# Optimization experiments

Hardware: AMD Instinct MI355X
Metric: run time of the kernel (lower is better)

## Reference

```python
import jax, jax.numpy as jnp
import numpy as np

B, S, H = 16, 4096, 1024

def setup_inputs() -> dict:
    key = jax.random.key(0)
    k1, k2, k3, k4, k5 = jax.random.split(key, 5)
    x = jax.random.normal(k1, (B, S, H), dtype=jnp.float32)
    lengths = jax.random.randint(k2, (B,), 1, S + 1, dtype=jnp.int32)
    W = jax.random.normal(k3, (H, H), dtype=jnp.float32) * (1.0 / np.sqrt(H))
    b = jax.random.normal(k4, (H,), dtype=jnp.float32) * 0.01
    key_vec = jax.random.normal(k5, (H,), dtype=jnp.float32)
    return {"x": x, "lengths": lengths, "W": W, "b": b, "key_vec": key_vec}

def reference(x, lengths, W, b, key_vec):
    # query = tanh(Linear(x)) : [B,S,H]
    query = jnp.tanh(jnp.einsum('bsh,oh->bso', x, W) + b)
    # scores = query @ key_vec : [B,S]
    scores = jnp.einsum('bsh,h->bs', query, key_vec)
    # masked softmax over valid positions (equivalent to per-sample slice softmax)
    seq_len = x.shape[1]
    valid = jnp.arange(seq_len)[None, :] < lengths[:, None]  # [B,S]
    scores = jnp.where(valid, scores, -jnp.inf)
    attn = jax.nn.softmax(scores, axis=-1)  # masked positions get 0
    # weighted sum of x : [B,H]
    return jnp.einsum('bs,bsh->bh', attn, x)
```

## Files before the change

### kernel.cpp

```cpp
#include <hip/hip_runtime.h>
#include <math.h>

#define BB 16
#define SS 4096
#define HH 1024
#define SCH 64


typedef __attribute__((ext_vector_type(8))) short bf16x8;
typedef __attribute__((ext_vector_type(16))) float f32x16;

__device__ __forceinline__ void gl_lds16(const void* g, void* l) {
  __builtin_amdgcn_global_load_lds(
      (const __attribute__((address_space(1))) void*)g,
      (__attribute__((address_space(3))) void*)l, 16, 0, 0);
}

__global__ __launch_bounds__(256) void conv_w(const float* __restrict__ W,
                                              unsigned short* __restrict__ Bbuf) {
  int ct = blockIdx.x, kc = blockIdx.y;
  unsigned short* blk = Bbuf + (size_t)(ct * 32 + kc) * 8192;
  int tid = threadIdx.x;
#pragma unroll
  for (int it = 0; it < 16; ++it) {
    int flat = it * 256 + tid;
    int n = flat >> 5, kk = flat & 31;
    float f = W[(size_t)(ct * 128 + n) * HH + kc * 32 + kk];
    unsigned u = __float_as_uint(f);
    float hf = __uint_as_float(u & 0xffff0000u);
    blk[n * 32 + kk] = (unsigned short)(u >> 16);
    blk[4096 + n * 32 + kk] = (unsigned short)(__float_as_uint(f - hf) >> 16);
  }
}

__global__ __launch_bounds__(256, 2) void scores_gemm(
    const float* __restrict__ x, const int* __restrict__ lengths,
    const unsigned short* __restrict__ Bbuf, const float* __restrict__ bias,
    const float* __restrict__ key, float* __restrict__ scores) {
  int ct = blockIdx.x;
  int t = blockIdx.y;
  int b = t >> 5;
  int s0 = (t & 31) * 128;
  if (s0 >= lengths[b]) return;

  __shared__ char lds[32768];
  int tid = threadIdx.x;
  int lane = tid & 63, w = tid >> 6;
  int wm = w & 1, wn = w >> 1;

  f32x16 acc[2][2];
#pragma unroll
  for (int mt = 0; mt < 2; ++mt)
#pragma unroll
    for (int nt = 0; nt < 2; ++nt)
#pragma unroll
      for (int i = 0; i < 16; ++i) acc[mt][nt][i] = 0.f;

  const float* xb = x + ((size_t)b * SS + s0) * HH;
  const char* Bblk0 = (const char*)Bbuf + (size_t)ct * 32 * 16384;

  int ar = tid >> 3;
  int ak = (tid & 7) * 4;

  int mrow = lane & 31;
  int khsel = lane >> 5;
  char* aP = lds + (wm * 64 + mrow) * 64 + khsel * 16;
  char* bP = lds + 16384 + (wn * 64 + mrow) * 64 + khsel * 16;

  for (int kc = 0; kc < 32; ++kc) {
    const char* Bblk = Bblk0 + kc * 16384;
#pragma unroll
    for (int i = 0; i < 4; ++i) {
      int c = w * 4 + i;
      gl_lds16(Bblk + c * 1024 + lane * 16, lds + 16384 + c * 1024);
    }
#pragma unroll
    for (int it = 0; it < 4; ++it) {
      int r = ar + it * 32;
      float4 v = *(const float4*)(xb + (size_t)r * HH + kc * 32 + ak);
      unsigned u0 = __float_as_uint(v.x), u1 = __float_as_uint(v.y);
      unsigned u2 = __float_as_uint(v.z), u3 = __float_as_uint(v.w);
      float l0 = v.x - __uint_as_float(u0 & 0xffff0000u);
      float l1 = v.y - __uint_as_float(u1 & 0xffff0000u);
      float l2 = v.z - __uint_as_float(u2 & 0xffff0000u);
      float l3 = v.w - __uint_as_float(u3 & 0xffff0000u);
      uint2 hp, lp;
      hp.x = (u0 >> 16) | (u1 & 0xffff0000u);
      hp.y = (u2 >> 16) | (u3 & 0xffff0000u);
      lp.x = (__float_as_uint(l0) >> 16) | (__float_as_uint(l1) & 0xffff0000u);
      lp.y = (__float_as_uint(l2) >> 16) | (__float_as_uint(l3) & 0xffff0000u);
      *(uint2*)(lds + r * 64 + ak * 2) = hp;
      *(uint2*)(lds + 8192 + r * 64 + ak * 2) = lp;
    }
    __syncthreads();

#pragma unroll
    for (int kh = 0; kh < 2; ++kh) {
      bf16x8 ah[2], al[2], bh[2], bl[2];
#pragma unroll
      for (int mt = 0; mt < 2; ++mt) {
        ah[mt] = *(bf16x8*)(aP + mt * 2048 + kh * 32);
        al[mt] = *(bf16x8*)(aP + 8192 + mt * 2048 + kh * 32);
        bh[mt] = *(bf16x8*)(bP + mt * 2048 + kh * 32);
        bl[mt] = *(bf16x8*)(bP + 8192 + mt * 2048 + kh * 32);
      }
#pragma unroll
      for (int mt = 0; mt < 2; ++mt)
#pragma unroll
        for (int nt = 0; nt < 2; ++nt) {
          acc[mt][nt] = __builtin_amdgcn_mfma_f32_32x32x16_bf16(
              ah[mt], bh[nt], acc[mt][nt], 0, 0, 0);
          acc[mt][nt] = __builtin_amdgcn_mfma_f32_32x32x16_bf16(
              ah[mt], bl[nt], acc[mt][nt], 0, 0, 0);
          acc[mt][nt] = __builtin_amdgcn_mfma_f32_32x32x16_bf16(
              al[mt], bh[nt], acc[mt][nt], 0, 0, 0);
        }
    }
    __syncthreads();
  }

  int col = lane & 31;
  int rbase = (lane >> 5) * 4;
  float bo[2], ko[2];
#pragma unroll
  for (int nt = 0; nt < 2; ++nt) {
    int o = ct * 128 + wn * 64 + nt * 32 + col;
    bo[nt] = bias[o];
    ko[nt] = key[o];
  }
  float* srow = scores + (size_t)b * SS + s0;
#pragma unroll
  for (int mt = 0; mt < 2; ++mt) {
#pragma unroll
    for (int reg = 0; reg < 16; ++reg) {
      float sv = tanhf(acc[mt][0][reg] + bo[0]) * ko[0] +
                 tanhf(acc[mt][1][reg] + bo[1]) * ko[1];
#pragma unroll
      for (int off = 1; off < 32; off <<= 1) sv += __shfl_xor(sv, off);
      if (col == 0) {
        int row = wm * 64 + mt * 32 + (reg & 3) + 8 * (reg >> 2) + rbase;
        atomicAdd(srow + row, sv);
      }
    }
  }
}

__global__ __launch_bounds__(256) void softmax_kernel(float* __restrict__ sc,
                                                      const int* __restrict__ lengths) {
  int b = blockIdx.x;
  int L = lengths[b];
  float* p = sc + (size_t)b * SS;
  __shared__ float sred[34];
  int tid = threadIdx.x;

  float m = -3.0e38f;
  for (int s = tid; s < L; s += 256) m = fmaxf(m, p[s]);
  for (int off = 32; off > 0; off >>= 1) m = fmaxf(m, __shfl_down(m, off));
  if ((tid & 63) == 0) sred[tid >> 6] = m;
  __syncthreads();
  if (tid == 0) {
    float mm = sred[0];
    for (int w = 1; w < 4; ++w) mm = fmaxf(mm, sred[w]);
    sred[32] = mm;
  }
  __syncthreads();
  m = sred[32];

  float z = 0.f;
  for (int s = tid; s < L; s += 256) z += expf(p[s] - m);
  for (int off = 32; off > 0; off >>= 1) z += __shfl_down(z, off);
  if ((tid & 63) == 0) sred[tid >> 6] = z;
  __syncthreads();
  if (tid == 0) {
    float zz = 0.f;
    for (int w = 0; w < 4; ++w) zz += sred[w];
    sred[33] = zz;
  }
  __syncthreads();
  float inv = 1.f / sred[33];
  for (int s = tid; s < L; s += 256) p[s] = expf(p[s] - m) * inv;
}

__global__ __launch_bounds__(256) void wsum_kernel(const float* __restrict__ x,
                                                   const float* __restrict__ p,
                                                   const int* __restrict__ lengths,
                                                   float* __restrict__ out) {
  int b = blockIdx.y;
  int L = lengths[b];
  int sbeg = blockIdx.x * SCH;
  if (sbeg >= L) return;
  int send = min(sbeg + SCH, L);
  int h = threadIdx.x * 4;
  const float* xb = x + (size_t)b * SS * HH;
  const float* pb = p + (size_t)b * SS;
  float4 acc = {0.f, 0.f, 0.f, 0.f};
  for (int s = sbeg; s < send; ++s) {
    float wgt = pb[s];
    float4 v = *(const float4*)(xb + (size_t)s * HH + h);
    acc.x = fmaf(wgt, v.x, acc.x);
    acc.y = fmaf(wgt, v.y, acc.y);
    acc.z = fmaf(wgt, v.z, acc.z);
    acc.w = fmaf(wgt, v.w, acc.w);
  }
  float* o = out + (size_t)b * HH + h;
  atomicAdd(o + 0, acc.x);
  atomicAdd(o + 1, acc.y);
  atomicAdd(o + 2, acc.z);
  atomicAdd(o + 3, acc.w);
}

extern "C" void kernel_launch(void* const* d_in, const int* in_sizes, int n_in,
                              void* d_out, int out_size, void* d_ws, size_t ws_size,
                              hipStream_t stream) {
  const float* x = (const float*)d_in[0];
  const int* lengths = (const int*)d_in[1];
  const float* W = (const float*)d_in[2];
  const float* bias = (const float*)d_in[3];
  const float* key = (const float*)d_in[4];
  float* out = (float*)d_out;

  unsigned short* Bbuf = (unsigned short*)d_ws;
  float* scores = (float*)((char*)d_ws + (size_t)4 * 1024 * 1024);

  hipMemsetAsync(d_out, 0, (size_t)out_size * sizeof(float), stream);
  hipMemsetAsync(scores, 0, (size_t)BB * SS * sizeof(float), stream);
  conv_w<<<dim3(8, 32), 256, 0, stream>>>(W, Bbuf);
  scores_gemm<<<dim3(8, 512), 256, 0, stream>>>(x, lengths, Bbuf, bias, key, scores);
  softmax_kernel<<<dim3(BB), 256, 0, stream>>>(scores, lengths);
  wsum_kernel<<<dim3(SS / SCH, BB), 256, 0, stream>>>(x, scores, lengths, out);
}
```

Baseline: 637.5 us.

## Double-buffer GEMM LDS with XOR swizzle, regroup blocks, tune softmax and wsum

The scores GEMM now double-buffers its A and B tiles in a 64KB LDS. The next k-chunk's global loads are issued before the current chunk's MFMA compute. Both tiles use an XOR swizzle, applied also to the preconverted W layout, to avoid LDS bank conflicts. Block indices are remapped so that blocks sharing x rows run close together, for L2 reuse. Softmax uses 1024 threads and stores the exps instead of recomputing them, and wsum unrolls the sequence loop by 8 with vector weight loads. Doubling LDS per block may reduce occupancy.

```diff
diff --git a/kernel.cpp b/kernel.cpp
--- a/kernel.cpp
+++ b/kernel.cpp
@@ -28,8 +28,10 @@
     float f = W[(size_t)(ct * 128 + n) * HH + kc * 32 + kk];
     unsigned u = __float_as_uint(f);
     float hf = __uint_as_float(u & 0xffff0000u);
-    blk[n * 32 + kk] = (unsigned short)(u >> 16);
-    blk[4096 + n * 32 + kk] = (unsigned short)(__float_as_uint(f - hf) >> 16);
+    int slot = (kk >> 3) ^ ((n >> 1) & 3);
+    int idx = n * 32 + slot * 8 + (kk & 7);
+    blk[idx] = (unsigned short)(u >> 16);
+    blk[4096 + idx] = (unsigned short)(__float_as_uint(f - hf) >> 16);
   }
 }
 
@@ -37,13 +39,20 @@
     const float* __restrict__ x, const int* __restrict__ lengths,
     const unsigned short* __restrict__ Bbuf, const float* __restrict__ bias,
     const float* __restrict__ key, float* __restrict__ scores) {
-  int ct = blockIdx.x;
-  int t = blockIdx.y;
+  int f = blockIdx.y * 8 + blockIdx.x;
+  int r8 = f & 7, j = f >> 3;
+  int t = r8 + (j & ~7);
+  int ct = j & 7;
   int b = t >> 5;
   int s0 = (t & 31) * 128;
   if (s0 >= lengths[b]) return;
 
-  __shared__ char lds[32768];
+  __shared__ char lds[65536];
+  char* A0 = lds;
+  char* B0 = lds + 16384;
+  char* A1 = lds + 32768;
+  char* B1 = lds + 49152;
+
   int tid = threadIdx.x;
   int lane = tid & 63, w = tid >> 6;
   int wm = w & 1, wn = w >> 1;
@@ -60,64 +69,92 @@
   const char* Bblk0 = (const char*)Bbuf + (size_t)ct * 32 * 16384;
 
   int ar = tid >> 3;
-  int ak = (tid & 7) * 4;
+  int ak8 = tid & 7;
+  int awoff = (((ak8 >> 1) ^ ((ar >> 1) & 3)) << 4) + ((ak8 & 1) << 3);
 
   int mrow = lane & 31;
   int khsel = lane >> 5;
-  char* aP = lds + (wm * 64 + mrow) * 64 + khsel * 16;
-  char* bP = lds + 16384 + (wn * 64 + mrow) * 64 + khsel * 16;
-
-  for (int kc = 0; kc < 32; ++kc) {
-    const char* Bblk = Bblk0 + kc * 16384;
-#pragma unroll
-    for (int i = 0; i < 4; ++i) {
-      int c = w * 4 + i;
-      gl_lds16(Bblk + c * 1024 + lane * 16, lds + 16384 + c * 1024);
-    }
-#pragma unroll
-    for (int it = 0; it < 4; ++it) {
-      int r = ar + it * 32;
-      float4 v = *(const float4*)(xb + (size_t)r * HH + kc * 32 + ak);
-      unsigned u0 = __float_as_uint(v.x), u1 = __float_as_uint(v.y);
-      unsigned u2 = __float_as_uint(v.z), u3 = __float_as_uint(v.w);
-      float l0 = v.x - __uint_as_float(u0 & 0xffff0000u);
-      float l1 = v.y - __uint_as_float(u1 & 0xffff0000u);
-      float l2 = v.z - __uint_as_float(u2 & 0xffff0000u);
-      float l3 = v.w - __uint_as_float(u3 & 0xffff0000u);
-      uint2 hp, lp;
-      hp.x = (u0 >> 16) | (u1 & 0xffff0000u);
-      hp.y = (u2 >> 16) | (u3 & 0xffff0000u);
-      lp.x = (__float_as_uint(l0) >> 16) | (__float_as_uint(l1) & 0xffff0000u);
-      lp.y = (__float_as_uint(l2) >> 16) | (__float_as_uint(l3) & 0xffff0000u);
-      *(uint2*)(lds + r * 64 + ak * 2) = hp;
-      *(uint2*)(lds + 8192 + r * 64 + ak * 2) = lp;
-    }
+  int rx = (mrow >> 1) & 3;
+  int soff0 = ((khsel ^ rx)) << 4;
+  int soff1 = (((2 + khsel) ^ rx)) << 4;
+  int rbA = (wm * 64 + mrow) * 64;
+  int rbB = (wn * 64 + mrow) * 64;
+
+  float4 v[4];
+
+#define STAGE_ISSUE(KC, BDST)                                              \
+  {                                                                        \
+    const char* Bblk = Bblk0 + (KC) * 16384;                               \
+    _Pragma("unroll") for (int i = 0; i < 4; ++i) {                        \
+      int c = w * 4 + i;                                                   \
+      gl_lds16(Bblk + c * 1024 + lane * 16, (BDST) + c * 1024);            \
+    }                                                                      \
+    _Pragma("unroll") for (int it = 0; it < 4; ++it)                       \
+      v[it] = *(const float4*)(xb + (size_t)(ar + it * 32) * HH +          \
+                               (KC) * 32 + ak8 * 4);                       \
+  }
+
+#define A_WRITE(ADST)                                                      \
+  {                                                                        \
+    _Pragma("unroll") for (int it = 0; it < 4; ++it) {                     \
+      int rr = ar + it * 32;                                               \
+      unsigned u0 = __float_as_uint(v[it].x), u1 = __float_as_uint(v[it].y);\
+      unsigned u2 = __float_as_uint(v[it].z), u3 = __float_as_uint(v[it].w);\
+      float l0 = v[it].x - __uint_as_float(u0 & 0xffff0000u);              \
+      float l1 = v[it].y - __uint_as_float(u1 & 0xffff0000u);              \
+      float l2 = v[it].z - __uint_as_float(u2 & 0xffff0000u);              \
+      float l3 = v[it].w - __uint_as_float(u3 & 0xffff0000u);              \
+      uint2 hp, lp;                                                        \
+      hp.x = (u0 >> 16) | (u1 & 0xffff0000u);                              \
+      hp.y = (u2 >> 16) | (u3 & 0xffff0000u);                              \
+      lp.x = (__float_as_uint(l0) >> 16) | (__float_as_uint(l1) & 0xffff0000u);\
+      lp.y = (__float_as_uint(l2) >> 16) | (__float_as_uint(l3) & 0xffff0000u);\
+      *(uint2*)((ADST) + rr * 64 + awoff) = hp;                            \
+      *(uint2*)((ADST) + 8192 + rr * 64 + awoff) = lp;                     \
+    }                                                                      \
+  }
+
+#define COMPUTE(AC, BC)                                                    \
+  {                                                                        \
+    _Pragma("unroll") for (int kh = 0; kh < 2; ++kh) {                     \
+      int so = kh ? soff1 : soff0;                                         \
+      bf16x8 ah[2], al[2], bh[2], bl[2];                                   \
+      _Pragma("unroll") for (int mt = 0; mt < 2; ++mt) {                   \
+        ah[mt] = *(bf16x8*)((AC) + rbA + mt * 2048 + so);                  \
+        al[mt] = *(bf16x8*)((AC) + 8192 + rbA + mt * 2048 + so);           \
+        bh[mt] = *(bf16x8*)((BC) + rbB + mt * 2048 + so);                  \
+        bl[mt] = *(bf16x8*)((BC) + 8192 + rbB + mt * 2048 + so);           \
+      }                                                                    \
+      _Pragma("unroll") for (int mt = 0; mt < 2; ++mt)                     \
+        _Pragma("unroll") for (int nt = 0; nt < 2; ++nt) {                 \
+          acc[mt][nt] = __builtin_amdgcn_mfma_f32_32x32x16_bf16(           \
+              ah[mt], bh[nt], acc[mt][nt], 0, 0, 0);                       \
+          acc[mt][nt] = __builtin_amdgcn_mfma_f32_32x32x16_bf16(           \
+              ah[mt], bl[nt], acc[mt][nt], 0, 0, 0);                       \
+          acc[mt][nt] = __builtin_amdgcn_mfma_f32_32x32x16_bf16(           \
+              al[mt], bh[nt], acc[mt][nt], 0, 0, 0);                       \
+        }                                                                  \
+    }                                                                      \
+  }
+
+  STAGE_ISSUE(0, B0)
+  A_WRITE(A0)
+  __syncthreads();
+
+  for (int kc = 0; kc < 32; kc += 2) {
+    STAGE_ISSUE(kc + 1, B1)
+    COMPUTE(A0, B0)
+    A_WRITE(A1)
     __syncthreads();
-
-#pragma unroll
-    for (int kh = 0; kh < 2; ++kh) {
-      bf16x8 ah[2], al[2], bh[2], bl[2];
-#pragma unroll
-      for (int mt = 0; mt < 2; ++mt) {
-        ah[mt] = *(bf16x8*)(aP + mt * 2048 + kh * 32);
-        al[mt] = *(bf16x8*)(aP + 8192 + mt * 2048 + kh * 32);
-        bh[mt] = *(bf16x8*)(bP + mt * 2048 + kh * 32);
-        bl[mt] = *(bf16x8*)(bP + 8192 + mt * 2048 + kh * 32);
-      }
-#pragma unroll
-      for (int mt = 0; mt < 2; ++mt)
-#pragma unroll
-        for (int nt = 0; nt < 2; ++nt) {
-          acc[mt][nt] = __builtin_amdgcn_mfma_f32_32x32x16_bf16(
-              ah[mt], bh[nt], acc[mt][nt], 0, 0, 0);
-          acc[mt][nt] = __builtin_amdgcn_mfma_f32_32x32x16_bf16(
-              ah[mt], bl[nt], acc[mt][nt], 0, 0, 0);
-          acc[mt][nt] = __builtin_amdgcn_mfma_f32_32x32x16_bf16(
-              al[mt], bh[nt], acc[mt][nt], 0, 0, 0);
-        }
-    }
+    if (kc + 2 < 32) { STAGE_ISSUE(kc + 2, B0) }
+    COMPUTE(A1, B1)
+    if (kc + 2 < 32) { A_WRITE(A0) }
     __syncthreads();
   }
+
+#undef STAGE_ISSUE
+#undef A_WRITE
+#undef COMPUTE
 
   int col = lane & 31;
   int rbase = (lane >> 5) * 4;
@@ -145,40 +182,44 @@
   }
 }
 
-__global__ __launch_bounds__(256) void softmax_kernel(float* __restrict__ sc,
-                                                      const int* __restrict__ lengths) {
+__global__ __launch_bounds__(1024) void softmax_kernel(float* __restrict__ sc,
+                                                       const int* __restrict__ lengths) {
   int b = blockIdx.x;
   int L = lengths[b];
   float* p = sc + (size_t)b * SS;
-  __shared__ float sred[34];
+  __shared__ float sred[18];
   int tid = threadIdx.x;
 
   float m = -3.0e38f;
-  for (int s = tid; s < L; s += 256) m = fmaxf(m, p[s]);
+  for (int s = tid; s < L; s += 1024) m = fmaxf(m, p[s]);
   for (int off = 32; off > 0; off >>= 1) m = fmaxf(m, __shfl_down(m, off));
   if ((tid & 63) == 0) sred[tid >> 6] = m;
   __syncthreads();
   if (tid == 0) {
     float mm = sred[0];
-    for (int w = 1; w < 4; ++w) mm = fmaxf(mm, sred[w]);
-    sred[32] = mm;
-  }
-  __syncthreads();
-  m = sred[32];
+    for (int w = 1; w < 16; ++w) mm = fmaxf(mm, sred[w]);
+    sred[16] = mm;
+  }
+  __syncthreads();
+  m = sred[16];
 
   float z = 0.f;
-  for (int s = tid; s < L; s += 256) z += expf(p[s] - m);
+  for (int s = tid; s < L; s += 1024) {
+    float e = expf(p[s] - m);
+    p[s] = e;
+    z += e;
+  }
   for (int off = 32; off > 0; off >>= 1) z += __shfl_down(z, off);
   if ((tid & 63) == 0) sred[tid >> 6] = z;
   __syncthreads();
   if (tid == 0) {
     float zz = 0.f;
-    for (int w = 0; w < 4; ++w) zz += sred[w];
-    sred[33] = zz;
-  }
-  __syncthreads();
-  float inv = 1.f / sred[33];
-  for (int s = tid; s < L; s += 256) p[s] = expf(p[s] - m) * inv;
+    for (int w = 0; w < 16; ++w) zz += sred[w];
+    sred[17] = zz;
+  }
+  __syncthreads();
+  float inv = 1.f / sred[17];
+  for (int s = tid; s < L; s += 1024) p[s] *= inv;
 }
 
 __global__ __launch_bounds__(256) void wsum_kernel(const float* __restrict__ x,
@@ -191,16 +232,33 @@
   if (sbeg >= L) return;
   int send = min(sbeg + SCH, L);
   int h = threadIdx.x * 4;
-  const float* xb = x + (size_t)b * SS * HH;
+  const float* xb = x + (size_t)b * SS * HH + h;
   const float* pb = p + (size_t)b * SS;
   float4 acc = {0.f, 0.f, 0.f, 0.f};
-  for (int s = sbeg; s < send; ++s) {
+  int s = sbeg;
+  for (; s + 8 <= send; s += 8) {
+    float4 pa = *(const float4*)(pb + s);
+    float4 pc = *(const float4*)(pb + s + 4);
+    float4 vv[8];
+#pragma unroll
+    for (int jj = 0; jj < 8; ++jj)
+      vv[jj] = *(const float4*)(xb + (size_t)(s + jj) * HH);
+    float pw[8] = {pa.x, pa.y, pa.z, pa.w, pc.x, pc.y, pc.z, pc.w};
+#pragma unroll
+    for (int jj = 0; jj < 8; ++jj) {
+      acc.x = fmaf(pw[jj], vv[jj].x, acc.x);
+      acc.y = fmaf(pw[jj], vv[jj].y, acc.y);
+      acc.z = fmaf(pw[jj], vv[jj].z, acc.z);
+      acc.w = fmaf(pw[jj], vv[jj].w, acc.w);
+    }
+  }
+  for (; s < send; ++s) {
     float wgt = pb[s];
-    float4 v = *(const float4*)(xb + (size_t)s * HH + h);
-    acc.x = fmaf(wgt, v.x, acc.x);
-    acc.y = fmaf(wgt, v.y, acc.y);
-    acc.z = fmaf(wgt, v.z, acc.z);
-    acc.w = fmaf(wgt, v.w, acc.w);
+    float4 vx = *(const float4*)(xb + (size_t)s * HH);
+    acc.x = fmaf(wgt, vx.x, acc.x);
+    acc.y = fmaf(wgt, vx.y, acc.y);
+    acc.z = fmaf(wgt, vx.z, acc.z);
+    acc.w = fmaf(wgt, vx.w, acc.w);
   }
   float* o = out + (size_t)b * HH + h;
   atomicAdd(o + 0, acc.x);
@@ -226,6 +284,6 @@
   hipMemsetAsync(scores, 0, (size_t)BB * SS * sizeof(float), stream);
   conv_w<<<dim3(8, 32), 256, 0, stream>>>(W, Bbuf);
   scores_gemm<<<dim3(8, 512), 256, 0, stream>>>(x, lengths, Bbuf, bias, key, scores);
-  softmax_kernel<<<dim3(BB), 256, 0, stream>>>(scores, lengths);
+  softmax_kernel<<<dim3(BB), 1024, 0, stream>>>(scores, lengths);
   wsum_kernel<<<dim3(SS / SCH, BB), 256, 0, stream>>>(x, scores, lengths, out);
 }
```

After: 581.6 us. 1.1x faster.
